# Performance work log

Measured on AMD Instinct MI355X. Metric: run time of the kernel, lower is better.

The kernel has to match this reference:

```python
import jax, jax.numpy as jnp
import numpy as np

EPS = 1e-5  # torch BatchNorm2d default eps
NUM_PIXELS = 2  # M_Relax window
GROUPS = 4


def conv2d(x, w, b, groups, pad):
    y = jax.lax.conv_general_dilated(
        x, w, window_strides=(1, 1), padding=[(pad, pad), (pad, pad)],
        dimension_numbers=('NCHW', 'OIHW', 'NCHW'), feature_group_count=groups)
    return y + b[None, :, None, None]


def batchnorm(x, gamma, beta):
    # training-mode BN: batch statistics over (N,H,W)
    mean = jnp.mean(x, axis=(0, 2, 3), keepdims=True)
    var = jnp.var(x, axis=(0, 2, 3), keepdims=True)
    return gamma[None, :, None, None] * (x - mean) * jax.lax.rsqrt(var + EPS) + beta[None, :, None, None]


def resb(x, w1, b1, w2, b2):
    y = conv2d(x, w1, b1, GROUPS, 1)
    y = jnp.where(y > 0, y, 0.1 * y)  # LeakyReLU(0.1)
    y = conv2d(y, w2, b2, GROUPS, 1)
    return y + x


def m_relax(M, n=NUM_PIXELS):
    # sum of M shifted by -n..n along the query (row) axis with zero padding
    out = M
    for i in range(1, n + 1):
        out = out + jnp.pad(M[:, :-i, :], ((0, 0), (i, 0), (0, 0)))
        out = out + jnp.pad(M[:, i:, :], ((0, 0), (0, i), (0, 0)))
    return out


def reference(x_left, x_right, bn_gamma, bn_beta, rb_w1, rb_b1, rb_w2, rb_b2, q_w, q_b, k_w, k_b):
    b, c, h, w = x_left.shape
    Q = conv2d(resb(batchnorm(x_left, bn_gamma, bn_beta), rb_w1, rb_b1, rb_w2, rb_b2), q_w, q_b, GROUPS, 0)
    K = conv2d(resb(batchnorm(x_right, bn_gamma, bn_beta), rb_w1, rb_b1, rb_w2, rb_b2), k_w, k_b, GROUPS, 0)
    Q = Q - jnp.mean(Q, axis=3, keepdims=True)
    K = K - jnp.mean(K, axis=3, keepdims=True)
    # rows of each image attend across width: [b*h, w, c]
    Qr = Q.transpose(0, 2, 3, 1).reshape(b * h, w, c)
    Kr = K.transpose(0, 2, 3, 1).reshape(b * h, w, c)
    score = jnp.einsum('nuc,nvc->nuv', Qr, Kr)  # [b*h, w, w]
    M_rl = jax.nn.softmax(score, axis=-1)               # right->left
    M_lr = jax.nn.softmax(score.transpose(0, 2, 1), axis=-1)  # left->right
    # validity maps (detached in original)
    V_left = jax.lax.stop_gradient(jnp.einsum('nuv,nvu->nu', m_relax(M_rl), M_lr)).reshape(b, 1, h, w)
    V_right = jax.lax.stop_gradient(jnp.einsum('nuv,nvu->nu', m_relax(M_lr), M_rl)).reshape(b, 1, h, w)
    Vl = jnp.tanh(5.0 * V_left)
    Vr = jnp.tanh(5.0 * V_right)
    xr_rows = x_right.transpose(0, 2, 3, 1).reshape(b * h, w, c)
    xl_rows = x_left.transpose(0, 2, 3, 1).reshape(b * h, w, c)
    x_leftT = jnp.einsum('nuv,nvc->nuc', M_rl, xr_rows).reshape(b, h, w, c).transpose(0, 3, 1, 2)
    x_rightT = jnp.einsum('nuv,nvc->nuc', M_lr, xl_rows).reshape(b, h, w, c).transpose(0, 3, 1, 2)
    out_left = x_left * (1 - Vl) + x_leftT * Vl
    out_right = x_right * (1 - Vr) + x_rightT * Vr
    return out_left, out_right


def setup_inputs() -> dict:
    key = jax.random.key(0)
    ks = jax.random.split(key, 12)
    b, c, h, w = 8, 64, 128, 128
    cg = c // GROUPS
    s_conv3 = 0.1
    return {
        'x_left': jax.random.normal(ks[0], (b, c, h, w), jnp.float32),
        'x_right': jax.random.normal(ks[1], (b, c, h, w), jnp.float32),
        'bn_gamma': jnp.ones((c,), jnp.float32),
        'bn_beta': jnp.zeros((c,), jnp.float32),
        'rb_w1': jax.random.normal(ks[2], (c, cg, 3, 3), jnp.float32) * s_conv3,
        'rb_b1': jax.random.normal(ks[3], (c,), jnp.float32) * 0.01,
        'rb_w2': jax.random.normal(ks[4], (c, cg, 3, 3), jnp.float32) * s_conv3,
        'rb_b2': jax.random.normal(ks[5], (c,), jnp.float32) * 0.01,
        'q_w': jax.random.normal(ks[6], (c, cg, 1, 1), jnp.float32) * 0.2,
        'q_b': jax.random.normal(ks[7], (c,), jnp.float32) * 0.01,
        'k_w': jax.random.normal(ks[8], (c, cg, 1, 1), jnp.float32) * 0.2,
        'k_b': jax.random.normal(ks[9], (c,), jnp.float32) * 0.01,
    }
```

## Files before the change

kernel.cpp:

```cpp
#include <hip/hip_runtime.h>

#define CH_N 64
#define HH 128
#define WW 128
#define BB 8
#define HW (HH*WW)

__global__ __launch_bounds__(256) void k_stats(const float* __restrict__ xL,
                                               const float* __restrict__ xR,
                                               float* __restrict__ sums) {
  int blk = blockIdx.x;
  int img = blk >> 8, c = (blk >> 2) & 63, s = blk & 3;
  const float* x = img ? xR : xL;
  float sm = 0.f, sq = 0.f;
  for (int n = 2*s; n < 2*s+2; ++n) {
    const float4* p = (const float4*)(x + ((size_t)(n*64+c))*HW);
    for (int i = threadIdx.x; i < 4096; i += 256) {
      float4 v = p[i];
      sm += (v.x+v.y)+(v.z+v.w);
      sq += (v.x*v.x+v.y*v.y)+(v.z*v.z+v.w*v.w);
    }
  }
  #pragma unroll
  for (int o = 32; o > 0; o >>= 1) { sm += __shfl_down(sm, o); sq += __shfl_down(sq, o); }
  __shared__ float rs[2][4];
  int wid = threadIdx.x >> 6;
  if ((threadIdx.x & 63) == 0) { rs[0][wid] = sm; rs[1][wid] = sq; }
  __syncthreads();
  if (threadIdx.x == 0) {
    sm = (rs[0][0]+rs[0][1])+(rs[0][2]+rs[0][3]);
    sq = (rs[1][0]+rs[1][1])+(rs[1][2]+rs[1][3]);
    atomicAdd(&sums[(img*64+c)*2+0], sm);
    atomicAdd(&sums[(img*64+c)*2+1], sq);
  }
}

__global__ __launch_bounds__(128) void k_finalize(const float* __restrict__ sums,
                                                  const float* __restrict__ gamma,
                                                  const float* __restrict__ beta,
                                                  float* __restrict__ ss) {
  int t = threadIdx.x;
  if (t < 128) {
    int c = t & 63;
    float sm = sums[t*2], sq = sums[t*2+1];
    float mean = sm * (1.f/131072.f);
    float var  = sq * (1.f/131072.f) - mean*mean;
    float scale = gamma[c] * rsqrtf(var + 1e-5f);
    ss[t*2+0] = scale;
    ss[t*2+1] = beta[c] - mean*scale;
  }
}

#define WOFF  5824
#define QBOFF (WOFF + 256)

template<int MODE>
__global__ __launch_bounds__(256, 4) void k_conv(
    const float* __restrict__ inL, const float* __restrict__ inR,
    const float* __restrict__ xresL, const float* __restrict__ xresR,
    const float* __restrict__ w, const float* __restrict__ bias,
    const float* __restrict__ ss,
    float* __restrict__ outL_, float* __restrict__ outR_,
    const float* __restrict__ qwL, const float* __restrict__ qbL,
    const float* __restrict__ qwR, const float* __restrict__ qbR,
    float* __restrict__ rsL, float* __restrict__ rsR) {
  __shared__ float smem[9024];
  int tile = blockIdx.x, g = blockIdx.y, nz = blockIdx.z;
  int img = nz >> 3, n = nz & 7;
  const float* in   = img ? inR : inL;
  const float* xres = img ? xresR : xresL;
  const float* ssp  = ss + img*128;
  float* out        = img ? outR_ : outL_;
  const float* qw1  = img ? qwR : qwL;
  const float* qb1  = img ? qbR : qbL;
  float* rowsum     = img ? rsR : rsL;

  int x0 = (tile & 7) << 4, y0 = (tile >> 3) << 4;
  int t = threadIdx.x;
  int n64 = n*64 + g*16;

  {
    int ocw = t >> 4, icw = t & 15;
    const float* wp = w + (size_t)(g*16 + ocw)*144 + icw*9;
    float* wd = &smem[WOFF + ocw*200 + icw*12];
    #pragma unroll
    for (int k = 0; k < 9; ++k) wd[k] = wp[k];
  }

  {
    int q = t & 3, ry = ((t >> 2) & 15) + 1, icb = t >> 6;
    int gy = y0 + ry - 1;
    const float* rowp = in + ((size_t)(n64 + icb)*128 + gy)*128 + x0 + (q << 2);
    float* dst = &smem[icb*364 + ry*20 + 4 + (q << 2)];
    #pragma unroll
    for (int k = 0; k < 4; ++k) {
      float4 v4 = *(const float4*)(rowp + (size_t)(4*k)*HW);
      if (MODE == 0) {
        int cc = (g*16 + icb + 4*k) * 2;
        float sA = ssp[cc], sB = ssp[cc+1];
        v4.x = fmaf(v4.x,sA,sB); v4.y = fmaf(v4.y,sA,sB);
        v4.z = fmaf(v4.z,sA,sB); v4.w = fmaf(v4.w,sA,sB);
      }
      *(float4*)(dst + 4*k*364) = v4;
    }
  }
  if (t < 64) {
    int side = t >> 5, lane = t & 31;
    int ic = lane >> 1, half = lane & 1;
    int gx = side ? x0 + 16 : x0 - 1;
    bool xok = ((unsigned)gx < 128u);
    int gxc = xok ? gx : 0;
    int col = side ? 20 : 3;
    const float* base = in + (size_t)(n64 + ic)*HW;
    float sA = 0.f, sB = 0.f;
    if (MODE == 0) { int cc = (g*16+ic)*2; sA = ssp[cc]; sB = ssp[cc+1]; }
    #pragma unroll
    for (int k = 0; k < 9; ++k) {
      int r = half*9 + k;
      int gy = y0 - 1 + r;
      bool ok = xok && ((unsigned)gy < 128u);
      int gyc = ((unsigned)gy < 128u) ? gy : 0;
      float v = base[(size_t)gyc*128 + gxc];
      if (MODE == 0) v = fmaf(v, sA, sB);
      smem[ic*364 + r*20 + col] = ok ? v : 0.f;
    }
  } else if (t < 192) {
    int j = t - 64;
    int half = j >> 6, l = j & 63;
    int ic = l >> 2, q = l & 3;
    int gy = half ? y0 + 16 : y0 - 1;
    bool ok = ((unsigned)gy < 128u);
    int gyc = ok ? gy : 0;
    float4 v4 = *(const float4*)&in[((size_t)(n64 + ic)*128 + gyc)*128 + x0 + (q << 2)];
    if (MODE == 0) {
      int cc = (g*16+ic)*2;
      float sA = ssp[cc], sB = ssp[cc+1];
      v4.x = fmaf(v4.x,sA,sB); v4.y = fmaf(v4.y,sA,sB);
      v4.z = fmaf(v4.z,sA,sB); v4.w = fmaf(v4.w,sA,sB);
    }
    if (!ok) { v4.x = 0.f; v4.y = 0.f; v4.z = 0.f; v4.w = 0.f; }
    int ry = half ? 17 : 0;
    *(float4*)&smem[ic*364 + ry*20 + 4 + (q << 2)] = v4;
  }
  __syncthreads();

  int oc = t >> 4, sub = t & 15;
  int sy = (sub >> 2) << 2, sx = (sub & 3) << 2;
  int c = g*16 + oc;
  float acc[4][4];
  float bv = bias[c];
  #pragma unroll
  for (int i = 0; i < 4; ++i)
    #pragma unroll
    for (int j = 0; j < 4; ++j) acc[i][j] = bv;

  for (int ic = 0; ic < 16; ++ic) {
    const float* it = &smem[ic*364 + sy*20 + sx];
    float win[6][6];
    #pragma unroll
    for (int r = 0; r < 6; ++r) {
      const float* rp = it + r*20;
      float lw = rp[3];
      const float4 m4 = *(const float4*)(rp + 4);
      float rw = rp[8];
      win[r][0]=lw; win[r][1]=m4.x; win[r][2]=m4.y;
      win[r][3]=m4.z; win[r][4]=m4.w; win[r][5]=rw;
    }
    const float4 w0 = *(const float4*)&smem[WOFF + oc*200 + ic*12];
    const float4 w1 = *(const float4*)&smem[WOFF + oc*200 + ic*12 + 4];
    const float  w8 = smem[WOFF + oc*200 + ic*12 + 8];
    float wv[9] = {w0.x,w0.y,w0.z,w0.w,w1.x,w1.y,w1.z,w1.w,w8};
    #pragma unroll
    for (int i = 0; i < 4; ++i)
      #pragma unroll
      for (int j = 0; j < 4; ++j) {
        float a = acc[i][j];
        #pragma unroll
        for (int ky = 0; ky < 3; ++ky)
          #pragma unroll
          for (int kx = 0; kx < 3; ++kx)
            a = fmaf(win[i+ky][j+kx], wv[ky*3+kx], a);
        acc[i][j] = a;
      }
  }

  if (MODE == 0) {
    #pragma unroll
    for (int i = 0; i < 4; ++i) {
      int oy = y0 + sy + i;
      size_t rowbase = ((size_t)(n*64+c)*128 + oy)*128;
      float4 o;
      o.x = acc[i][0] > 0.f ? acc[i][0] : 0.1f*acc[i][0];
      o.y = acc[i][1] > 0.f ? acc[i][1] : 0.1f*acc[i][1];
      o.z = acc[i][2] > 0.f ? acc[i][2] : 0.1f*acc[i][2];
      o.w = acc[i][3] > 0.f ? acc[i][3] : 0.1f*acc[i][3];
      *(float4*)&out[rowbase + x0 + sx] = o;
    }
  } else {
    float sA = ssp[c*2], sB = ssp[c*2+1];
    __syncthreads();
    #pragma unroll
    for (int i = 0; i < 4; ++i) {
      int oy = y0 + sy + i;
      size_t rowbase = ((size_t)(n*64+c)*128 + oy)*128;
      const float4 xr4 = *(const float4*)&xres[rowbase + x0 + sx];
      float4 v4;
      v4.x = acc[i][0] + fmaf(xr4.x, sA, sB);
      v4.y = acc[i][1] + fmaf(xr4.y, sA, sB);
      v4.z = acc[i][2] + fmaf(xr4.z, sA, sB);
      v4.w = acc[i][3] + fmaf(xr4.w, sA, sB);
      *(float4*)&smem[oc*328 + (sy+i)*20 + sx] = v4;
    }
    smem[WOFF + t] = qw1[g*256 + t];
    if (t < 16) smem[QBOFF + t] = qb1[g*16 + t];
    __syncthreads();

    float qa[4][4];
    float bq = smem[QBOFF + oc];
    #pragma unroll
    for (int i = 0; i < 4; ++i)
      #pragma unroll
      for (int j = 0; j < 4; ++j) qa[i][j] = bq;
    #pragma unroll 4
    for (int ic = 0; ic < 16; ++ic) {
      float wq = smem[WOFF + oc*16 + ic];
      #pragma unroll
      for (int i = 0; i < 4; ++i) {
        const float4 yv = *(const float4*)&smem[ic*328 + (sy+i)*20 + sx];
        qa[i][0] = fmaf(wq, yv.x, qa[i][0]);
        qa[i][1] = fmaf(wq, yv.y, qa[i][1]);
        qa[i][2] = fmaf(wq, yv.z, qa[i][2]);
        qa[i][3] = fmaf(wq, yv.w, qa[i][3]);
      }
    }
    #pragma unroll
    for (int i = 0; i < 4; ++i) {
      int oy = y0 + sy + i;
      size_t rowbase = ((size_t)(n*64+c)*128 + oy)*128;
      float4 o4 = make_float4(qa[i][0], qa[i][1], qa[i][2], qa[i][3]);
      *(float4*)&out[rowbase + x0 + sx] = o4;
      float r = (qa[i][0]+qa[i][1]) + (qa[i][2]+qa[i][3]);
      r += __shfl_xor(r, 1);
      r += __shfl_xor(r, 2);
      if ((t & 3) == 0) atomicAdd(&rowsum[(size_t)(n*64+c)*128 + oy], r);
    }
  }
}

__device__ __forceinline__ int SW(int r, int c) {
  return (r << 7) + (((c >> 2) ^ (r & 31)) << 2) + (c & 3);
}
__device__ __forceinline__ int SWQ(int r, int q) {
  return (r << 7) + ((q ^ (r & 31)) << 2);
}

__global__ __launch_bounds__(512, 4) void k_pam(const float* __restrict__ Q,
                                                const float* K,
                                                const float* __restrict__ XL,
                                                const float* __restrict__ XR,
                                                float* __restrict__ outL,
                                                float* outR,
                                                const float* __restrict__ rsL,
                                                const float* __restrict__ rsR) {
  extern __shared__ float smp[];
  float* ST   = smp;
  float* CHB  = smp + 16384;
  float* rmax = smp + 18432;
  float* rinv = rmax + 128;
  float* cmax = rmax + 256;
  float* cinv = rmax + 384;
  float* Vl   = rmax + 512;
  float* Vr   = rmax + 640;
  float* Pu   = rmax + 768;
  float* Qv   = rmax + 896;
  float* ms   = rmax + 1024;
  float* pm   = CHB;
  float* pl   = CHB + 512;
  float* pm2  = CHB + 1024;
  float* pl2  = CHB + 1536;

  int t = threadIdx.x;
  int b = blockIdx.x >> 7, h = blockIdx.x & 127;
  size_t qbase = ((size_t)(b*64)*128 + h)*128;

  {
    int u0 = (t & 31) << 2, v0 = (t >> 5) << 3;
    float a0[8], a1[8], a2[8], a3[8];
    #pragma unroll
    for (int j = 0; j < 8; ++j) { a0[j]=0.f; a1[j]=0.f; a2[j]=0.f; a3[j]=0.f; }
    int half = t >> 8;
    int cl_ld = (t >> 5) & 7;
    int u4_ld = (t & 31) << 2;
    const float* src = half ? K : Q;
    const float* rsum = half ? rsR : rsL;
    float mean = rsum[((size_t)b*64 + cl_ld)*128 + h] * (1.f/128.f);
    float4 v = *(const float4*)&src[qbase + (size_t)cl_ld*HW + u4_ld];
    for (int cb = 0; cb < 8; ++cb) {
      __syncthreads();
      v.x -= mean; v.y -= mean; v.z -= mean; v.w -= mean;
      *(float4*)&CHB[half*1024 + cl_ld*128 + u4_ld] = v;
      if (cb < 7) {
        mean = rsum[((size_t)b*64 + (cb+1)*8 + cl_ld)*128 + h] * (1.f/128.f);
        v = *(const float4*)&src[qbase + (size_t)((cb+1)*8 + cl_ld)*HW + u4_ld];
      }
      __syncthreads();
      #pragma unroll
      for (int cl = 0; cl < 8; ++cl) {
        const float4 qv = *(const float4*)&CHB[cl*128 + u0];
        const float4 k0 = *(const float4*)&CHB[1024 + cl*128 + v0];
        const float4 k1 = *(const float4*)&CHB[1024 + cl*128 + v0 + 4];
        float kk[8] = {k0.x,k0.y,k0.z,k0.w,k1.x,k1.y,k1.z,k1.w};
        #pragma unroll
        for (int j = 0; j < 8; ++j) {
          float kv = kk[j];
          a0[j] = fmaf(qv.x, kv, a0[j]);
          a1[j] = fmaf(qv.y, kv, a1[j]);
          a2[j] = fmaf(qv.z, kv, a2[j]);
          a3[j] = fmaf(qv.w, kv, a3[j]);
        }
      }
    }
    #pragma unroll
    for (int j = 0; j < 8; ++j) {
      int r = v0 + j;
      *(float4*)&ST[SWQ(r, u0 >> 2)] = make_float4(a0[j], a1[j], a2[j], a3[j]);
    }
  }
  __syncthreads();

  {
    int u = t & 127, q = t >> 7, vb = q << 5;
    float m = -1e30f;
    for (int v = vb; v < vb+32; ++v) m = fmaxf(m, ST[SW(v, u)]);
    float l = 0.f;
    for (int v = vb; v < vb+32; ++v) l += __expf(ST[SW(v, u)] - m);
    float m2 = -1e30f;
    for (int k = (vb >> 2); k < (vb >> 2) + 8; ++k) {
      const float4 x4 = *(const float4*)&ST[SWQ(u, k)];
      m2 = fmaxf(m2, fmaxf(fmaxf(x4.x, x4.y), fmaxf(x4.z, x4.w)));
    }
    float l2 = 0.f;
    for (int k = (vb >> 2); k < (vb >> 2) + 8; ++k) {
      const float4 x4 = *(const float4*)&ST[SWQ(u, k)];
      l2 += (__expf(x4.x-m2)+__expf(x4.y-m2)) + (__expf(x4.z-m2)+__expf(x4.w-m2));
    }
    pm[t] = m; pl[t] = l;
    pm2[t] = m2; pl2[t] = l2;
  }
  __syncthreads();
  if (t < 256) {
    int u = t & 127;
    const float* PM = (t < 128) ? pm : pm2;
    const float* PL = (t < 128) ? pl : pl2;
    float m = fmaxf(fmaxf(PM[u], PM[128+u]), fmaxf(PM[256+u], PM[384+u]));
    float l = PL[u]*__expf(PM[u]-m) + PL[128+u]*__expf(PM[128+u]-m)
            + PL[256+u]*__expf(PM[256+u]-m) + PL[384+u]*__expf(PM[384+u]-m);
    if (t < 128) { rmax[u] = m; rinv[u] = 1.f/l; }
    else         { cmax[u] = m; cinv[u] = 1.f/l; }
  }
  __syncthreads();

  if (t < 64) {
    float m = fmaxf(rmax[t], rmax[t+64]);
    #pragma unroll
    for (int o = 32; o > 0; o >>= 1) m = fmaxf(m, __shfl_down(m, o));
    if (t == 0) ms[0] = m;
  }
  __syncthreads();

  {
    float ms0 = ms[0];
    if (t < 128)      Pu[t] = __expf(rmax[t] - ms0) / rinv[t];
    else if (t < 256) { int v = t - 128; Qv[v] = __expf(ms0 - cmax[v]) * cinv[v]; }
    int u = t & 127, q = t >> 7;
    float ru = rmax[u], ri = rinv[u];
    for (int v = (q << 5); v < (q << 5) + 32; ++v) {
      int a = SW(v, u);
      ST[a] = __expf(ST[a] - ru) * ri;
    }
  }
  __syncthreads();

  {
    int u = t & 127, q = t >> 7, vb = q << 5;
    int rcl[5]; float wL[5], qvd[5];
    #pragma unroll
    for (int d = 0; d < 5; ++d) {
      int uu = u - 2 + d;
      bool ok = (uu >= 0 && uu < 128);
      rcl[d] = ok ? uu : u;
      wL[d]  = ok ? 1.f : 0.f;
      qvd[d] = ok ? Qv[uu] : 0.f;
    }
    float pu_u = Pu[u];
    float accL = 0.f, accR = 0.f;
    for (int v = vb; v < vb+32; ++v) {
      float rr0 = ST[SW(v, rcl[0])], rr1 = ST[SW(v, rcl[1])];
      float rr2 = ST[SW(v, u)];
      float rr3 = ST[SW(v, rcl[3])], rr4 = ST[SW(v, rcl[4])];
      float R = rr2 + (wL[0]*rr0 + wL[1]*rr1) + (wL[3]*rr3 + wL[4]*rr4);
      accL = fmaf(R * rr2, Qv[v], accL);
    }
    accL *= pu_u;
    {
      int ush = u >> 3;
      #pragma unroll 2
      for (int a = 0; a < 8; ++a) {
        #pragma unroll
        for (int bq = 0; bq < 4; ++bq) {
          int v = vb + (a << 2) + ((bq + ush) & 3);
          float cc0 = ST[SW(rcl[0], v)], cc1 = ST[SW(rcl[1], v)];
          float cc2 = ST[SW(u, v)];
          float cc3 = ST[SW(rcl[3], v)], cc4 = ST[SW(rcl[4], v)];
          float G = cc2*qvd[2] + (cc0*qvd[0] + cc1*qvd[1]) + (cc3*qvd[3] + cc4*qvd[4]);
          accR = fmaf(G * cc2, Pu[v], accR);
        }
      }
    }
    __syncthreads();
    pm[t] = accL; pl[t] = accR;
  }
  __syncthreads();
  if (t < 128) {
    float vsL = pm[t]+pm[128+t]+pm[256+t]+pm[384+t];
    float vsR = pl[t]+pl[128+t]+pl[256+t]+pl[384+t];
    Vl[t] = tanhf(5.f*vsL);
    Vr[t] = tanhf(5.f*vsR);
  }

  int ul = t & 63, c0 = (t >> 6) << 3;
  int c_ld = t >> 3, q_ld = (t & 7) << 2;
  int csw_st = c_ld ^ (((q_ld >> 2) & 7) << 3);

  {
    float acc0[8], acc1[8];
    #pragma unroll
    for (int j = 0; j < 8; ++j) { acc0[j]=0.f; acc1[j]=0.f; }
    float4 r4 = *(const float4*)&XR[qbase + (size_t)c_ld*HW + q_ld];
    for (int cb = 0; cb < 4; ++cb) {
      __syncthreads();
      CHB[(q_ld+0)*64+csw_st] = r4.x; CHB[(q_ld+1)*64+csw_st] = r4.y;
      CHB[(q_ld+2)*64+csw_st] = r4.z; CHB[(q_ld+3)*64+csw_st] = r4.w;
      if (cb < 3)
        r4 = *(const float4*)&XR[qbase + (size_t)c_ld*HW + ((cb+1) << 5) + q_ld];
      __syncthreads();
      int vb = cb << 5;
      for (int vv = 0; vv < 32; ++vv) {
        int v = vb + vv;
        float m0 = ST[SW(v, ul)];
        float m1 = ST[SW(v, ul+64)];
        int cs = c0 ^ (((vv >> 2) & 7) << 3);
        const float4 xa = *(const float4*)&CHB[vv*64 + cs];
        const float4 xb = *(const float4*)&CHB[vv*64 + cs + 4];
        acc0[0]=fmaf(m0,xa.x,acc0[0]); acc0[1]=fmaf(m0,xa.y,acc0[1]);
        acc0[2]=fmaf(m0,xa.z,acc0[2]); acc0[3]=fmaf(m0,xa.w,acc0[3]);
        acc0[4]=fmaf(m0,xb.x,acc0[4]); acc0[5]=fmaf(m0,xb.y,acc0[5]);
        acc0[6]=fmaf(m0,xb.z,acc0[6]); acc0[7]=fmaf(m0,xb.w,acc0[7]);
        acc1[0]=fmaf(m1,xa.x,acc1[0]); acc1[1]=fmaf(m1,xa.y,acc1[1]);
        acc1[2]=fmaf(m1,xa.z,acc1[2]); acc1[3]=fmaf(m1,xa.w,acc1[3]);
        acc1[4]=fmaf(m1,xb.x,acc1[4]); acc1[5]=fmaf(m1,xb.y,acc1[5]);
        acc1[6]=fmaf(m1,xb.z,acc1[6]); acc1[7]=fmaf(m1,xb.w,acc1[7]);
      }
    }
    float vl0 = Vl[ul], vl1 = Vl[ul+64];
    #pragma unroll
    for (int j = 0; j < 8; ++j) {
      size_t o0 = qbase + (size_t)(c0+j)*HW + ul;
      outL[o0]    = XL[o0]   *(1.f-vl0) + acc0[j]*vl0;
      outL[o0+64] = XL[o0+64]*(1.f-vl1) + acc1[j]*vl1;
    }
  }

  {
    float acc0[8], acc1[8];
    #pragma unroll
    for (int j = 0; j < 8; ++j) { acc0[j]=0.f; acc1[j]=0.f; }
    float qv_u0 = Qv[ul], qv_u1 = Qv[ul+64];
    float4 r4 = *(const float4*)&XL[qbase + (size_t)c_ld*HW + q_ld];
    for (int cb = 0; cb < 4; ++cb) {
      __syncthreads();
      CHB[(q_ld+0)*64+csw_st] = r4.x; CHB[(q_ld+1)*64+csw_st] = r4.y;
      CHB[(q_ld+2)*64+csw_st] = r4.z; CHB[(q_ld+3)*64+csw_st] = r4.w;
      if (cb < 3)
        r4 = *(const float4*)&XL[qbase + (size_t)c_ld*HW + ((cb+1) << 5) + q_ld];
      __syncthreads();
      int qb = cb << 3;
      for (int lq = 0; lq < 8; ++lq) {
        const float4 s0 = *(const float4*)&ST[SWQ(ul,    qb+lq)];
        const float4 s1 = *(const float4*)&ST[SWQ(ul+64, qb+lq)];
        const float4 pu4 = *(const float4*)&Pu[(qb+lq) << 2];
        float sv0[4] = {s0.x, s0.y, s0.z, s0.w};
        float sv1[4] = {s1.x, s1.y, s1.z, s1.w};
        float pv[4]  = {pu4.x, pu4.y, pu4.z, pu4.w};
        int cs = c0 ^ ((lq & 7) << 3);
        #pragma unroll
        for (int k = 0; k < 4; ++k) {
          float m0 = sv0[k] * pv[k] * qv_u0;
          float m1 = sv1[k] * pv[k] * qv_u1;
          const float4 xa0 = *(const float4*)&CHB[((lq<<2)+k)*64 + cs];
          const float4 xb0 = *(const float4*)&CHB[((lq<<2)+k)*64 + cs + 4];
          acc0[0]=fmaf(m0,xa0.x,acc0[0]); acc0[1]=fmaf(m0,xa0.y,acc0[1]);
          acc0[2]=fmaf(m0,xa0.z,acc0[2]); acc0[3]=fmaf(m0,xa0.w,acc0[3]);
          acc0[4]=fmaf(m0,xb0.x,acc0[4]); acc0[5]=fmaf(m0,xb0.y,acc0[5]);
          acc0[6]=fmaf(m0,xb0.z,acc0[6]); acc0[7]=fmaf(m0,xb0.w,acc0[7]);
          acc1[0]=fmaf(m1,xa0.x,acc1[0]); acc1[1]=fmaf(m1,xa0.y,acc1[1]);
          acc1[2]=fmaf(m1,xa0.z,acc1[2]); acc1[3]=fmaf(m1,xa0.w,acc1[3]);
          acc1[4]=fmaf(m1,xb0.x,acc1[4]); acc1[5]=fmaf(m1,xb0.y,acc1[5]);
          acc1[6]=fmaf(m1,xb0.z,acc1[6]); acc1[7]=fmaf(m1,xb0.w,acc1[7]);
        }
      }
    }
    float vr0 = Vr[ul], vr1 = Vr[ul+64];
    #pragma unroll
    for (int j = 0; j < 8; ++j) {
      size_t o0 = qbase + (size_t)(c0+j)*HW + ul;
      outR[o0]    = XR[o0]   *(1.f-vr0) + acc0[j]*vr0;
      outR[o0+64] = XR[o0+64]*(1.f-vr1) + acc1[j]*vr1;
    }
  }
}

extern "C" void kernel_launch(void* const* d_in, const int* in_sizes, int n_in,
                              void* d_out, int out_size, void* d_ws, size_t ws_size,
                              hipStream_t stream) {
  const float* xL    = (const float*)d_in[0];
  const float* xR    = (const float*)d_in[1];
  const float* gamma = (const float*)d_in[2];
  const float* beta  = (const float*)d_in[3];
  const float* rw1   = (const float*)d_in[4];
  const float* rb1   = (const float*)d_in[5];
  const float* rw2   = (const float*)d_in[6];
  const float* rb2   = (const float*)d_in[7];
  const float* qw    = (const float*)d_in[8];
  const float* qb    = (const float*)d_in[9];
  const float* kw    = (const float*)d_in[10];
  const float* kb    = (const float*)d_in[11];
  float* out = (float*)d_out;
  char* ws = (char*)d_ws;

  const size_t BUF = (size_t)BB*CH_N*HW*4;
  float* y1L  = (float*)(ws);
  float* y1R  = (float*)(ws + BUF);
  float* Qb   = (float*)(ws + 2*BUF);
  float* sums = (float*)(ws + 3*BUF);
  float* ss   = sums + 256;
  float* rsL  = sums + 512;
  float* rsR  = rsL + (size_t)BB*CH_N*HH;

  bool big = ws_size >= 4*BUF + (1u << 20);
  float* Kb = big ? (float*)(ws + 3*BUF + (1u << 20))
                  : (out + (size_t)BB*CH_N*HW);

  hipMemsetAsync(sums, 0, (512 + 2*(size_t)BB*CH_N*HH)*sizeof(float), stream);
  k_stats<<<512, 256, 0, stream>>>(xL, xR, sums);
  k_finalize<<<1, 128, 0, stream>>>(sums, gamma, beta, ss);

  dim3 cg(64, 4, 16);
  k_conv<0><<<cg, 256, 0, stream>>>(xL, xR, xL, xR, rw1, rb1, ss, y1L, y1R,
                                    nullptr, nullptr, nullptr, nullptr, nullptr, nullptr);
  k_conv<1><<<cg, 256, 0, stream>>>(y1L, y1R, xL, xR, rw2, rb2, ss, Qb, Kb,
                                    qw, qb, kw, kb, rsL, rsR);

  const int SMEM = 19464 * 4;
  hipFuncSetAttribute((const void*)k_pam, hipFuncAttributeMaxDynamicSharedMemorySize, SMEM);
  k_pam<<<1024, 512, SMEM, stream>>>(Qb, Kb, xL, xR, out, out + (size_t)BB*CH_N*HW, rsL, rsR);
}
```

Baseline: 487.6 us.

## Split second conv per image, reuse y1L buffer for K, remap blocks XCD-aware

Splits the second conv launch into separate left and right launches so K can be written into the y1L buffer, which is already consumed by the time the right-image launch runs. This drops the separate K buffer and its fallback into the output region. Block indices are remapped so that consecutive blocks (likely spread across XCDs) handle tiles of the same slice, aiming for better L2 locality. The change adds an extra launch and relies on in-order stream execution for the buffer aliasing to be safe.

```diff
diff --git a/kernel.cpp b/kernel.cpp
--- a/kernel.cpp
+++ b/kernel.cpp
@@ -62,18 +62,24 @@
     const float* __restrict__ ss,
     float* __restrict__ outL_, float* __restrict__ outR_,
     const float* __restrict__ qwL, const float* __restrict__ qbL,
-    const float* __restrict__ qwR, const float* __restrict__ qbR,
-    float* __restrict__ rsL, float* __restrict__ rsR) {
+    float* __restrict__ rsL) {
   __shared__ float smem[9024];
-  int tile = blockIdx.x, g = blockIdx.y, nz = blockIdx.z;
+  int l = blockIdx.x + (blockIdx.y << 6) + (blockIdx.z << 8);
+  int spx = (gridDim.y * gridDim.z) >> 3;
+  int jj = l >> 3;
+  int tile = jj & 63;
+  int slice = (l & 7) * spx + (jj >> 6);
+  int g = slice & 3;
+  int nz = slice >> 2;
+
   int img = nz >> 3, n = nz & 7;
   const float* in   = img ? inR : inL;
   const float* xres = img ? xresR : xresL;
   const float* ssp  = ss + img*128;
   float* out        = img ? outR_ : outL_;
-  const float* qw1  = img ? qwR : qwL;
-  const float* qb1  = img ? qbR : qbL;
-  float* rowsum     = img ? rsR : rsL;
+  const float* qw1  = qwL;
+  const float* qb1  = qbL;
+  float* rowsum     = rsL;
 
   int x0 = (tile & 7) << 4, y0 = (tile >> 3) << 4;
   int t = threadIdx.x;
@@ -126,8 +132,8 @@
     }
   } else if (t < 192) {
     int j = t - 64;
-    int half = j >> 6, l = j & 63;
-    int ic = l >> 2, q = l & 3;
+    int half = j >> 6, l2 = j & 63;
+    int ic = l2 >> 2, q = l2 & 3;
     int gy = half ? y0 + 16 : y0 - 1;
     bool ok = ((unsigned)gy < 128u);
     int gyc = ok ? gy : 0;
@@ -255,11 +261,11 @@
 }
 
 __global__ __launch_bounds__(512, 4) void k_pam(const float* __restrict__ Q,
-                                                const float* K,
+                                                const float* __restrict__ K,
                                                 const float* __restrict__ XL,
                                                 const float* __restrict__ XR,
                                                 float* __restrict__ outL,
-                                                float* outR,
+                                                float* __restrict__ outR,
                                                 const float* __restrict__ rsL,
                                                 const float* __restrict__ rsR) {
   extern __shared__ float smp[];
@@ -542,24 +548,24 @@
   float* y1L  = (float*)(ws);
   float* y1R  = (float*)(ws + BUF);
   float* Qb   = (float*)(ws + 2*BUF);
+  float* Kb   = y1L;
   float* sums = (float*)(ws + 3*BUF);
   float* ss   = sums + 256;
   float* rsL  = sums + 512;
   float* rsR  = rsL + (size_t)BB*CH_N*HH;
 
-  bool big = ws_size >= 4*BUF + (1u << 20);
-  float* Kb = big ? (float*)(ws + 3*BUF + (1u << 20))
-                  : (out + (size_t)BB*CH_N*HW);
-
   hipMemsetAsync(sums, 0, (512 + 2*(size_t)BB*CH_N*HH)*sizeof(float), stream);
   k_stats<<<512, 256, 0, stream>>>(xL, xR, sums);
   k_finalize<<<1, 128, 0, stream>>>(sums, gamma, beta, ss);
 
-  dim3 cg(64, 4, 16);
-  k_conv<0><<<cg, 256, 0, stream>>>(xL, xR, xL, xR, rw1, rb1, ss, y1L, y1R,
-                                    nullptr, nullptr, nullptr, nullptr, nullptr, nullptr);
-  k_conv<1><<<cg, 256, 0, stream>>>(y1L, y1R, xL, xR, rw2, rb2, ss, Qb, Kb,
-                                    qw, qb, kw, kb, rsL, rsR);
+  dim3 cg0(64, 4, 16);
+  k_conv<0><<<cg0, 256, 0, stream>>>(xL, xR, xL, xR, rw1, rb1, ss, y1L, y1R,
+                                     nullptr, nullptr, nullptr);
+  dim3 cg1(64, 4, 8);
+  k_conv<1><<<cg1, 256, 0, stream>>>(y1L, nullptr, xL, nullptr, rw2, rb2, ss,
+                                     Qb, nullptr, qw, qb, rsL);
+  k_conv<1><<<cg1, 256, 0, stream>>>(y1R, nullptr, xR, nullptr, rw2, rb2, ss + 128,
+                                     Kb, nullptr, kw, kb, rsR);
 
   const int SMEM = 19464 * 4;
   hipFuncSetAttribute((const void*)k_pam, hipFuncAttributeMaxDynamicSharedMemorySize, SMEM);
```

New measurement: 488.0 us. About the same (+0.1%).
